# Performance work log

Hardware: AMD Instinct MI355X
Metric: run time of the kernel (lower is better)

Reference implementation:

```python
import jax, jax.numpy as jnp
import numpy as np

EPS = 1e-4
LN_EPS = 1e-5  # torch LayerNorm default
N, E, IN_DIM, OUT_DIM = 100000, 800000, 128, 128


def setup_inputs() -> dict:
    key = jax.random.key(0)
    ks = jax.random.split(key, 8)
    s = 1.0 / np.sqrt(IN_DIM)
    return {
        "x": jax.random.normal(ks[0], (N, IN_DIM), dtype=jnp.float32),
        "edge_index": jax.random.randint(ks[1], (2, E), 0, N, dtype=jnp.int32),
        "degree": jax.random.randint(ks[2], (N,), 0, 16, dtype=jnp.int32),
        "W_fc": jax.random.normal(ks[3], (IN_DIM, OUT_DIM), dtype=jnp.float32) * s,
        "b_fc": jax.random.normal(ks[4], (OUT_DIM,), dtype=jnp.float32) * s,
        "W_rate": jax.random.normal(ks[5], (IN_DIM, OUT_DIM), dtype=jnp.float32) * s,
        "W_rob": jax.random.normal(ks[6], (IN_DIM, OUT_DIM), dtype=jnp.float32) * s,
        "b_rob": jax.random.normal(ks[7], (OUT_DIM,), dtype=jnp.float32) * s,
        "ln_gamma": jnp.ones((OUT_DIM,), dtype=jnp.float32),
        "ln_beta": jnp.zeros((OUT_DIM,), dtype=jnp.float32),
    }


def reference(x, edge_index, degree, W_fc, b_fc, W_rate, W_rob, b_rob, ln_gamma, ln_beta):
    n = x.shape[0]
    rate = jax.nn.softplus(x @ W_rate) + EPS            # [N, D_out]
    gamma = x @ W_rob + b_rob                           # [N, D_out]
    h = x @ W_fc + b_fc                                 # [N, D_out]
    row, col = edge_index[0], edge_index[1]
    msg = h[row] + h[col]                               # [E, D_out] gather-add
    agg = jax.ops.segment_sum(msg, row, num_segments=n) # scatter_sum over dst
    deg = degree.astype(x.dtype)[:, None]
    y = (rate * agg + gamma) / (1.0 + rate * deg + EPS)
    mean = jnp.mean(y, axis=-1, keepdims=True)
    var = jnp.var(y, axis=-1, keepdims=True)
    y = (y - mean) * jax.lax.rsqrt(var + LN_EPS) * ln_gamma + ln_beta
    return y  # act is Identity
```

## Files before the change

### kernel.cpp

```cpp
#include <hip/hip_runtime.h>
#include <hip/hip_bf16.h>
#include <math.h>

#define NN 100000
#define DIM 128
#define EPSF 1e-4f
#define LN_EPSF 1e-5f
#define XSTR 136
#define NTILES 3125
#define TPB 2
#define GEMM_GRID ((NTILES + TPB - 1) / TPB)
#define PACK_GRID ((NN + 255) / 256)
#define CAP 32

typedef float  floatx4 __attribute__((ext_vector_type(4)));
typedef float  floatx2 __attribute__((ext_vector_type(2)));
typedef short  shortx8 __attribute__((ext_vector_type(8)));

__device__ __forceinline__ ushort f2b(float f) {
    union { float f; unsigned u; } c; c.f = f;
    unsigned lsb = (c.u >> 16) & 1u;
    return (ushort)((c.u + 0x7fffu + lsb) >> 16);
}
__device__ __forceinline__ float b2f(ushort b) {
    union { unsigned u; float f; } c; c.u = ((unsigned)b) << 16;
    return c.f;
}
__device__ __forceinline__ unsigned pk2(float a, float b) {
    union { __hip_bfloat162 h2; unsigned u; } c;
    c.h2 = __float22bfloat162_rn(float2{a, b});
    return c.u;
}

__global__ __launch_bounds__(256) void pack_kernel(
    const float* __restrict__ Wfc, const float* __restrict__ Wrate,
    const float* __restrict__ Wrob, ushort* __restrict__ Bpack,
    int* __restrict__ cur)
{
    const int id = blockIdx.x * 256 + threadIdx.x;
    if (id < NN) cur[id] = 0;
    if (id >= 6144) return;
    const int lane = id & 63;
    const int ks   = (id >> 6) & 3;
    const int nt   = (id >> 8) & 7;
    const int w    = id >> 11;
    const float* W = (w == 0) ? Wfc : (w == 1) ? Wrate : Wrob;
    const int n  = nt * 16 + (lane & 15);
    const int kb = ks * 32 + (lane >> 4) * 8;
    ushort tmp[8];
#pragma unroll
    for (int j = 0; j < 8; ++j) tmp[j] = f2b(W[(kb + j) * DIM + n]);
    ushort* dst = Bpack + (size_t)id * 8;
#pragma unroll
    for (int j = 0; j < 8; ++j) dst[j] = tmp[j];
}

__global__ __launch_bounds__(256) void gemm3_mfma_kernel(
    const float* __restrict__ x,
    const ushort* __restrict__ Bpack,
    const float* __restrict__ bfc, const float* __restrict__ brob,
    ushort* __restrict__ h, ushort* __restrict__ rate, ushort* __restrict__ gam,
    const int* __restrict__ ei, int* __restrict__ cur,
    int* __restrict__ bucket, int E)
{
    __shared__ ushort xs[32 * XSTR];
    __shared__ ushort outb[3 * 32 * XSTR];
    const int tid  = threadIdx.x;
    const int wv   = tid >> 6;
    const int lane = tid & 63;

    for (int e = blockIdx.x * 512 + tid; e < E; e += GEMM_GRID * 512) {
#pragma unroll
        for (int q = 0; q < 2; ++q) {
            const int ee = e + q * 256;
            if (ee < E) {
                const int row = ei[ee];
                const int col = ei[E + ee];
                const int pos = atomicAdd(&cur[row], 1);
                if (pos < CAP) bucket[(size_t)row * CAP + pos] = col;
            }
        }
        break;
    }

    shortx8 bfrag[3][2][4];
#pragma unroll
    for (int w = 0; w < 3; ++w)
#pragma unroll
        for (int t = 0; t < 2; ++t) {
            const int nt = wv * 2 + t;
#pragma unroll
            for (int ks = 0; ks < 4; ++ks) {
                const ushort* p = Bpack + ((((size_t)w * 8 + nt) * 4 + ks) * 64 + lane) * 8;
                bfrag[w][t][ks] = *(const shortx8*)p;
            }
        }

    float4 bias_fc[2], bias_rob[2];
#pragma unroll
    for (int t = 0; t < 2; ++t) {
        const int colbase = wv * 32 + t * 16 + (lane >> 4) * 4;
        bias_fc[t]  = ((const float4*)bfc)[colbase >> 2];
        bias_rob[t] = ((const float4*)brob)[colbase >> 2];
    }

    const int tile0  = blockIdx.x * TPB;
    const int ntiles = (NTILES - tile0 < TPB) ? (NTILES - tile0) : TPB;

    {
        const size_t row0 = (size_t)tile0 * 32;
#pragma unroll
        for (int k = 0; k < 4; ++k) {
            const int i = tid + k * 256, r = i >> 5, c4 = i & 31;
            const float4 v = ((const float4*)(x + (row0 + r) * DIM))[c4];
            uint2 uu; uu.x = pk2(v.x, v.y); uu.y = pk2(v.z, v.w);
            *(uint2*)&xs[r * XSTR + c4 * 4] = uu;
        }
    }
    __syncthreads();

    for (int ti = 0; ti < ntiles; ++ti) {
        const size_t row0 = (size_t)(tile0 + ti) * 32;
        const bool hasnext = (ti + 1 < ntiles);

        float4 pf[4];
        if (hasnext) {
            const size_t nrow0 = row0 + 32;
#pragma unroll
            for (int k = 0; k < 4; ++k) {
                const int i = tid + k * 256, r = i >> 5, c4 = i & 31;
                pf[k] = ((const float4*)(x + (nrow0 + r) * DIM))[c4];
            }
        }

#pragma unroll
        for (int rt = 0; rt < 2; ++rt) {
            shortx8 af[4];
#pragma unroll
            for (int ks = 0; ks < 4; ++ks)
                af[ks] = *(const shortx8*)&xs[(rt * 16 + (lane & 15)) * XSTR
                                              + ks * 32 + (lane >> 4) * 8];
            floatx4 acc[3][2] = {};
#pragma unroll
            for (int ks = 0; ks < 4; ++ks)
#pragma unroll
                for (int w = 0; w < 3; ++w)
#pragma unroll
                    for (int t = 0; t < 2; ++t)
                        acc[w][t] = __builtin_amdgcn_mfma_f32_16x16x32_bf16(
                            bfrag[w][t][ks], af[ks], acc[w][t], 0, 0, 0);

            const int node = rt * 16 + (lane & 15);
#pragma unroll
            for (int t = 0; t < 2; ++t) {
                const int colbase = wv * 32 + t * 16 + (lane >> 4) * 4;
                {
                    uint2 st;
                    st.x = pk2(acc[0][t][0] + bias_fc[t].x, acc[0][t][1] + bias_fc[t].y);
                    st.y = pk2(acc[0][t][2] + bias_fc[t].z, acc[0][t][3] + bias_fc[t].w);
                    *(uint2*)&outb[0 * 32 * XSTR + node * XSTR + colbase] = st;
                }
                {
                    float rv[4];
#pragma unroll
                    for (int r = 0; r < 4; ++r) {
                        const float v = acc[1][t][r];
                        rv[r] = fmaxf(v, 0.f) + __logf(1.f + __expf(-fabsf(v))) + EPSF;
                    }
                    uint2 st; st.x = pk2(rv[0], rv[1]); st.y = pk2(rv[2], rv[3]);
                    *(uint2*)&outb[1 * 32 * XSTR + node * XSTR + colbase] = st;
                }
                {
                    uint2 st;
                    st.x = pk2(acc[2][t][0] + bias_rob[t].x, acc[2][t][1] + bias_rob[t].y);
                    st.y = pk2(acc[2][t][2] + bias_rob[t].z, acc[2][t][3] + bias_rob[t].w);
                    *(uint2*)&outb[2 * 32 * XSTR + node * XSTR + colbase] = st;
                }
            }
        }
        __syncthreads();

#pragma unroll
        for (int k = 0; k < 6; ++k) {
            const int w = k >> 1;
            const int rem = tid + (k & 1) * 256;
            const int node = rem >> 4, seg = rem & 15;
            const uint4 v = *(const uint4*)&outb[w * 32 * XSTR + node * XSTR + seg * 8];
            ushort* dstw = (w == 0) ? h : (w == 1) ? rate : gam;
            *(uint4*)(dstw + (row0 + node) * DIM + seg * 8) = v;
        }

        if (hasnext) {
#pragma unroll
            for (int k = 0; k < 4; ++k) {
                const int i = tid + k * 256, r = i >> 5, c4 = i & 31;
                uint2 uu; uu.x = pk2(pf[k].x, pf[k].y); uu.y = pk2(pf[k].z, pf[k].w);
                *(uint2*)&xs[r * XSTR + c4 * 4] = uu;
            }
        }
        __syncthreads();
    }
}

__global__ __launch_bounds__(256) void finalize_kernel(
    const ushort* __restrict__ h, const ushort* __restrict__ rate,
    const ushort* __restrict__ gam,
    const int* __restrict__ cur, const int* __restrict__ bucket,
    const int* __restrict__ degree,
    const float* __restrict__ ln_g, const float* __restrict__ ln_b,
    float* __restrict__ out)
{
    const int wave = threadIdx.x >> 6;
    const int lane = threadIdx.x & 63;
    const size_t rA = (size_t)blockIdx.x * 8 + wave * 2;
    const size_t rB = rA + 1;
    const unsigned* hu = (const unsigned*)h;

    const int   nA  = cur[rA],            nB  = cur[rB];
    const float dgA = (float)degree[rA],  dgB = (float)degree[rB];
    const int   bvA = bucket[rA * CAP + (lane & 31)];
    const int   bvB = bucket[rB * CAP + (lane & 31)];
    const unsigned hvA = hu[rA * 64 + lane],  hvB = hu[rB * 64 + lane];
    const unsigned rvA = ((const unsigned*)rate)[rA * 64 + lane];
    const unsigned rvB = ((const unsigned*)rate)[rB * 64 + lane];
    const unsigned gvA = ((const unsigned*)gam)[rA * 64 + lane];
    const unsigned gvB = ((const unsigned*)gam)[rB * 64 + lane];
    const float2 lg = ((const float2*)ln_g)[lane];
    const float2 lb = ((const float2*)ln_b)[lane];

    float axA = 0.f, ayA = 0.f, axB = 0.f, ayB = 0.f;
    const int mx = (nA > nB) ? nA : nB;
    for (int j = 0; j < mx; j += 8) {
        int cA[8], cB[8];
#pragma unroll
        for (int q = 0; q < 8; ++q) {
            cA[q] = __shfl(bvA, j + q, 64);
            cB[q] = __shfl(bvB, j + q, 64);
        }
        unsigned vA[8], vB[8];
#pragma unroll
        for (int q = 0; q < 8; ++q) {
            const int iA = (j + q < nA) ? cA[q] : (int)rA;
            const int iB = (j + q < nB) ? cB[q] : (int)rB;
            vA[q] = hu[(size_t)iA * 64 + lane];
            vB[q] = hu[(size_t)iB * 64 + lane];
        }
#pragma unroll
        for (int q = 0; q < 8; ++q) {
            if (j + q < nA) {
                axA += b2f((ushort)(vA[q] & 0xffff));
                ayA += b2f((ushort)(vA[q] >> 16));
            }
            if (j + q < nB) {
                axB += b2f((ushort)(vB[q] & 0xffff));
                ayB += b2f((ushort)(vB[q] >> 16));
            }
        }
    }

#pragma unroll
    for (int rr = 0; rr < 2; ++rr) {
        const size_t row = rr ? rB : rA;
        const float cn = (float)(rr ? nB : nA);
        const float dg = rr ? dgB : dgA;
        const unsigned hv = rr ? hvB : hvA;
        const unsigned rv = rr ? rvB : rvA;
        const unsigned gv = rr ? gvB : gvA;
        const float ax = rr ? axB : axA, ay = rr ? ayB : ayA;

        const float h0 = b2f((ushort)(hv & 0xffff)), h1 = b2f((ushort)(hv >> 16));
        const float r0 = b2f((ushort)(rv & 0xffff)), r1 = b2f((ushort)(rv >> 16));
        const float g0 = b2f((ushort)(gv & 0xffff)), g1 = b2f((ushort)(gv >> 16));

        const float a0 = cn * h0 + ax;
        const float a1 = cn * h1 + ay;
        const float y0 = (r0 * a0 + g0) / (1.f + r0 * dg + EPSF);
        const float y1 = (r1 * a1 + g1) / (1.f + r1 * dg + EPSF);

        float s  = y0 + y1;
        float s2 = y0 * y0 + y1 * y1;
#pragma unroll
        for (int o = 32; o > 0; o >>= 1) {
            s  += __shfl_xor(s,  o, 64);
            s2 += __shfl_xor(s2, o, 64);
        }
        const float mean = s * (1.f / 128.f);
        const float var  = s2 * (1.f / 128.f) - mean * mean;
        const float inv  = rsqrtf(var + LN_EPSF);

        floatx2 o;
        o.x = (y0 - mean) * inv * lg.x + lb.x;
        o.y = (y1 - mean) * inv * lg.y + lb.y;
        __builtin_nontemporal_store(o, (floatx2*)(out + row * DIM) + lane);
    }
}

extern "C" void kernel_launch(void* const* d_in, const int* in_sizes, int n_in,
                              void* d_out, int out_size, void* d_ws, size_t ws_size,
                              hipStream_t stream)
{
    const float* x      = (const float*)d_in[0];
    const int*   ei     = (const int*)  d_in[1];
    const int*   degree = (const int*)  d_in[2];
    const float* Wfc    = (const float*)d_in[3];
    const float* bfc    = (const float*)d_in[4];
    const float* Wrate  = (const float*)d_in[5];
    const float* Wrob   = (const float*)d_in[6];
    const float* brob   = (const float*)d_in[7];
    const float* ln_g   = (const float*)d_in[8];
    const float* ln_b   = (const float*)d_in[9];
    float* out = (float*)d_out;

    const int E = in_sizes[1] / 2;
    const size_t NEL = (size_t)NN * DIM;

    ushort* h     = (ushort*)d_ws;
    ushort* rate  = h + NEL;
    ushort* gam   = rate + NEL;
    ushort* Bpack = gam + NEL;
    int*   cur    = (int*)(Bpack + 49152);
    int*   bucket = cur + NN;

    pack_kernel<<<PACK_GRID, 256, 0, stream>>>(Wfc, Wrate, Wrob, Bpack, cur);
    gemm3_mfma_kernel<<<GEMM_GRID, 256, 0, stream>>>(x, Bpack, bfc, brob,
                                                     h, rate, gam,
                                                     ei, cur, bucket, E);
    finalize_kernel<<<NN / 8, 256, 0, stream>>>(h, rate, gam, cur, bucket,
                                                degree, ln_g, ln_b, out);
}
```

Baseline: 214.8 us.

## Split edge bucketing into separate fill kernel and use nontemporal loads in finalize

Moves the atomic edge-bucket fill out of the GEMM kernel into its own fill_kernel launched between pack and GEMM, which removes the atomic traffic from the MFMA kernel's prologue. It also switches the finalize kernel's single-use reads (counts, degree, buckets, rate, gamma) to nontemporal loads so they do not push the reused h rows out of cache. The cost is one extra kernel launch and the loss of overlap between the fill and the GEMM work.

```diff
diff --git a/kernel.cpp b/kernel.cpp
--- a/kernel.cpp
+++ b/kernel.cpp
@@ -11,6 +11,7 @@
 #define TPB 2
 #define GEMM_GRID ((NTILES + TPB - 1) / TPB)
 #define PACK_GRID ((NN + 255) / 256)
+#define FILL_GRID 1563
 #define CAP 32
 
 typedef float  floatx4 __attribute__((ext_vector_type(4)));
@@ -55,33 +56,40 @@
     for (int j = 0; j < 8; ++j) dst[j] = tmp[j];
 }
 
+__global__ __launch_bounds__(256) void fill_kernel(
+    const int* __restrict__ ei, int* __restrict__ cur,
+    int* __restrict__ bucket, int E)
+{
+    const int base = blockIdx.x * 512 + threadIdx.x;
+#pragma unroll
+    for (int q = 0; q < 2; ++q) {
+        const int ee = base + q * 256;
+        if (ee < E) {
+            const int row = ei[ee];
+            const int col = ei[E + ee];
+            const int pos = atomicAdd(&cur[row], 1);
+            if (pos < CAP) bucket[(size_t)row * CAP + pos] = col;
+        }
+    }
+    for (int ee = base + 2 * FILL_GRID * 256; ee < E; ee += FILL_GRID * 512) {
+        const int row = ei[ee];
+        const int col = ei[E + ee];
+        const int pos = atomicAdd(&cur[row], 1);
+        if (pos < CAP) bucket[(size_t)row * CAP + pos] = col;
+    }
+}
+
 __global__ __launch_bounds__(256) void gemm3_mfma_kernel(
     const float* __restrict__ x,
     const ushort* __restrict__ Bpack,
     const float* __restrict__ bfc, const float* __restrict__ brob,
-    ushort* __restrict__ h, ushort* __restrict__ rate, ushort* __restrict__ gam,
-    const int* __restrict__ ei, int* __restrict__ cur,
-    int* __restrict__ bucket, int E)
+    ushort* __restrict__ h, ushort* __restrict__ rate, ushort* __restrict__ gam)
 {
     __shared__ ushort xs[32 * XSTR];
     __shared__ ushort outb[3 * 32 * XSTR];
     const int tid  = threadIdx.x;
     const int wv   = tid >> 6;
     const int lane = tid & 63;
-
-    for (int e = blockIdx.x * 512 + tid; e < E; e += GEMM_GRID * 512) {
-#pragma unroll
-        for (int q = 0; q < 2; ++q) {
-            const int ee = e + q * 256;
-            if (ee < E) {
-                const int row = ei[ee];
-                const int col = ei[E + ee];
-                const int pos = atomicAdd(&cur[row], 1);
-                if (pos < CAP) bucket[(size_t)row * CAP + pos] = col;
-            }
-        }
-        break;
-    }
 
     shortx8 bfrag[3][2][4];
 #pragma unroll
@@ -216,15 +224,17 @@
     const size_t rB = rA + 1;
     const unsigned* hu = (const unsigned*)h;
 
-    const int   nA  = cur[rA],            nB  = cur[rB];
-    const float dgA = (float)degree[rA],  dgB = (float)degree[rB];
-    const int   bvA = bucket[rA * CAP + (lane & 31)];
-    const int   bvB = bucket[rB * CAP + (lane & 31)];
+    const int   nA  = __builtin_nontemporal_load(&cur[rA]);
+    const int   nB  = __builtin_nontemporal_load(&cur[rB]);
+    const float dgA = (float)__builtin_nontemporal_load(&degree[rA]);
+    const float dgB = (float)__builtin_nontemporal_load(&degree[rB]);
+    const int   bvA = __builtin_nontemporal_load(&bucket[rA * CAP + (lane & 31)]);
+    const int   bvB = __builtin_nontemporal_load(&bucket[rB * CAP + (lane & 31)]);
     const unsigned hvA = hu[rA * 64 + lane],  hvB = hu[rB * 64 + lane];
-    const unsigned rvA = ((const unsigned*)rate)[rA * 64 + lane];
-    const unsigned rvB = ((const unsigned*)rate)[rB * 64 + lane];
-    const unsigned gvA = ((const unsigned*)gam)[rA * 64 + lane];
-    const unsigned gvB = ((const unsigned*)gam)[rB * 64 + lane];
+    const unsigned rvA = __builtin_nontemporal_load(&((const unsigned*)rate)[rA * 64 + lane]);
+    const unsigned rvB = __builtin_nontemporal_load(&((const unsigned*)rate)[rB * 64 + lane]);
+    const unsigned gvA = __builtin_nontemporal_load(&((const unsigned*)gam)[rA * 64 + lane]);
+    const unsigned gvB = __builtin_nontemporal_load(&((const unsigned*)gam)[rB * 64 + lane]);
     const float2 lg = ((const float2*)ln_g)[lane];
     const float2 lb = ((const float2*)ln_b)[lane];
 
@@ -322,9 +332,9 @@
     int*   bucket = cur + NN;
 
     pack_kernel<<<PACK_GRID, 256, 0, stream>>>(Wfc, Wrate, Wrob, Bpack, cur);
+    fill_kernel<<<FILL_GRID, 256, 0, stream>>>(ei, cur, bucket, E);
     gemm3_mfma_kernel<<<GEMM_GRID, 256, 0, stream>>>(x, Bpack, bfc, brob,
-                                                     h, rate, gam,
-                                                     ei, cur, bucket, E);
+                                                     h, rate, gam);
     finalize_kernel<<<NN / 8, 256, 0, stream>>>(h, rate, gam, cur, bucket,
                                                 degree, ln_g, ln_b, out);
 }
```

New measurement: 239.2 us. 11.4% more time.
